# Kernel tuning notes

Hardware: AMD Instinct MI355X
Metric: run time of the kernel (lower is better)

## Reference

```python
import jax, jax.numpy as jnp
import numpy as np

B, S, D, H, FF = 2, 2048, 512, 8, 2048
DK = D // H
EPS = 1e-5


def layer_norm(x, g, b):
    mu = jnp.mean(x, axis=-1, keepdims=True)
    var = jnp.mean((x - mu) ** 2, axis=-1, keepdims=True)
    return (x - mu) / jnp.sqrt(var + EPS) * g + b


def split_heads(x):  # [B,S,D] -> [B,H,S,DK]
    b, s, _ = x.shape
    return x.reshape(b, s, H, DK).transpose(0, 2, 1, 3)


def merge_heads(x):  # [B,H,S,DK] -> [B,S,D]
    b, h, s, dk = x.shape
    return x.transpose(0, 2, 1, 3).reshape(b, s, h * dk)


def mha(q_in, kv, in_w, in_b, out_w, out_b):
    # torch nn.MultiheadAttention, batch_first, eval mode (no dropout)
    Wq, Wk, Wv = in_w[:D], in_w[D:2 * D], in_w[2 * D:]
    bq, bk, bv = in_b[:D], in_b[D:2 * D], in_b[2 * D:]
    q = split_heads(q_in @ Wq.T + bq)
    k = split_heads(kv @ Wk.T + bk)
    v = split_heads(kv @ Wv.T + bv)
    scores = jnp.einsum('bhqd,bhkd->bhqk', q, k) / jnp.sqrt(jnp.float32(DK))
    attn = jax.nn.softmax(scores, axis=-1)
    out = merge_heads(jnp.einsum('bhqk,bhkd->bhqd', attn, v))
    return out @ out_w.T + out_b


def setup_inputs() -> dict:
    key = jax.random.key(0)
    ks = jax.random.split(key, 32)
    p = lambda k, shape: (jax.random.normal(k, shape, jnp.float32) * 0.02)
    inp = {
        'x_q': jax.random.normal(ks[0], (B, S, D), jnp.float32),
        'x1': jax.random.normal(ks[1], (B, S, D), jnp.float32),
        'x2': jax.random.normal(ks[2], (B, S, D), jnp.float32),
        # causal self-attention projections (no output proj in original)
        'sa_wq': p(ks[3], (D, D)), 'sa_bq': jnp.zeros((D,), jnp.float32),
        'sa_wk': p(ks[4], (D, D)), 'sa_bk': jnp.zeros((D,), jnp.float32),
        'sa_wv': p(ks[5], (D, D)), 'sa_bv': jnp.zeros((D,), jnp.float32),
        'ln1_g': jnp.ones((D,), jnp.float32), 'ln1_b': jnp.zeros((D,), jnp.float32),
        # shared cross-attention (cross_attn used twice in forward)
        'mha_in_w': p(ks[6], (3 * D, D)), 'mha_in_b': jnp.zeros((3 * D,), jnp.float32),
        'mha_out_w': p(ks[7], (D, D)), 'mha_out_b': jnp.zeros((D,), jnp.float32),
        # shared add_norm2 (used twice)
        'ln2_g': jnp.ones((D,), jnp.float32), 'ln2_b': jnp.zeros((D,), jnp.float32),
        # FFN
        'ffn_w1': p(ks[8], (FF, D)), 'ffn_b1': jnp.zeros((FF,), jnp.float32),
        'ffn_w2': p(ks[9], (D, FF)), 'ffn_b2': jnp.zeros((D,), jnp.float32),
        # add_norm3 (final)
        'ln3_g': jnp.ones((D,), jnp.float32), 'ln3_b': jnp.zeros((D,), jnp.float32),
    }
    return inp


def reference(x_q, x1, x2, sa_wq, sa_bq, sa_wk, sa_bk, sa_wv, sa_bv,
              ln1_g, ln1_b, mha_in_w, mha_in_b, mha_out_w, mha_out_b,
              ln2_g, ln2_b, ffn_w1, ffn_b1, ffn_w2, ffn_b2, ln3_g, ln3_b):
    # --- causal self-attention (hand-rolled, masked_fill with -1e9) ---
    q = split_heads(x_q @ sa_wq.T + sa_bq)
    k = split_heads(x_q @ sa_wk.T + sa_bk)
    v = split_heads(x_q @ sa_wv.T + sa_bv)
    scores = jnp.einsum('bhqd,bhkd->bhqk', q, k) / jnp.sqrt(jnp.float32(DK))
    causal = jnp.tril(jnp.ones((S, S), dtype=bool))
    scores = jnp.where(causal[None, None], scores, jnp.float32(-1e9))
    attn = jax.nn.softmax(scores, axis=-1)
    y_sa = merge_heads(jnp.einsum('bhqk,bhkd->bhqd', attn, v))
    y = layer_norm(x_q + y_sa, ln1_g, ln1_b)
    # --- cross-attention 1 (shared weights) + shared add_norm2 ---
    yattn = mha(y, x1, mha_in_w, mha_in_b, mha_out_w, mha_out_b)
    yattn = layer_norm(y + yattn, ln2_g, ln2_b)
    # --- cross-attention 2 (SAME module/weights as cross-attn 1) ---
    yattn2 = mha(yattn, x2, mha_in_w, mha_in_b, mha_out_w, mha_out_b)
    yattn2 = layer_norm(yattn + yattn2, ln2_g, ln2_b)
    # --- FFN + add_norm3 ---
    h = jax.nn.relu(yattn2 @ ffn_w1.T + ffn_b1)
    ff = h @ ffn_w2.T + ffn_b2
    return layer_norm(yattn2 + ff, ln3_g, ln3_b)
```

## Files before the change

### kernel.cpp

```cpp
#include <hip/hip_runtime.h>
#include <hip/hip_bf16.h>

#define S_LEN 2048
#define DMODEL 512
#define NHEAD 8
#define DKH 64
#define FFDIM 2048
#define BATCH 2
#define NROWS (BATCH * S_LEN)

using bf16 = __hip_bfloat16;
typedef __bf16 bf16x8 __attribute__((ext_vector_type(8)));
typedef float floatx4 __attribute__((ext_vector_type(4)));
typedef float floatx16 __attribute__((ext_vector_type(16)));

__device__ inline unsigned short f2bf_bits(float f) {
    union { float f; unsigned u; } c; c.f = f;
    return (unsigned short)((c.u + 0x7FFFu + ((c.u >> 16) & 1u)) >> 16);
}
__device__ inline unsigned pack2bf(float a, float b) {
    return (unsigned)f2bf_bits(a) | ((unsigned)f2bf_bits(b) << 16);
}
__device__ inline unsigned pk2(float a, float b) {
    float2 f; f.x = a; f.y = b;
    __hip_bfloat162 h = __float22bfloat162_rn(f);
    return *(unsigned*)&h;
}

__device__ __forceinline__ void gload_lds16(const bf16* g, bf16* l) {
    __builtin_amdgcn_global_load_lds(
        (const __attribute__((address_space(1))) void*)(const void*)g,
        (__attribute__((address_space(3))) void*)(void*)l, 16, 0, 0);
}

struct CvtSeg { const float* s; bf16* d; int n4; };
struct CvtDesc { CvtSeg seg[12]; };

__launch_bounds__(256)
__global__ void cvt_f32_bf16(CvtDesc desc) {
    const CvtSeg sg = desc.seg[blockIdx.y];
    const int stride = gridDim.x * 256;
    for (int i = blockIdx.x * 256 + threadIdx.x; i < sg.n4; i += stride) {
        const float4 v = ((const float4*)sg.s)[i];
        uint2 o;
        o.x = pack2bf(v.x, v.y);
        o.y = pack2bf(v.z, v.w);
        ((uint2*)sg.d)[i] = o;
    }
}

struct Epi {
    bf16*  outB[3];
    float* outF[3];
    const float* bias[3];
    float scale[3];
    int shift;
    int relu;
};

template <int BM, int BN>
__launch_bounds__(256)
__global__ void gemm2(const bf16* __restrict__ A, const bf16* __restrict__ W,
                      Epi epi, int K)
{
    constexpr int WR = BM / 32;
    constexpr int WC = BN / 32;
    constexpr int SA = BM / 16;
    constexpr int SB = BN / 16;
    constexpr int NG = 2 * (SA + SB);

    __shared__ alignas(16) bf16 As[2][BM][32];
    __shared__ alignas(16) bf16 Bs[2][BN][32];

    const int t = threadIdx.x;
    const int w = t >> 6;
    const int lane = t & 63;
    const int r16 = lane & 15;
    const int quad = lane >> 4;
    const int wm = w >> 1, wn = w & 1;
    const int m0 = blockIdx.x * BM;
    const int n0 = blockIdx.y * BN;

    floatx4 acc[WR][WC];
#pragma unroll
    for (int i = 0; i < WR; i++)
#pragma unroll
        for (int j = 0; j < WC; j++)
#pragma unroll
            for (int e = 0; e < 4; e++) acc[i][j][e] = 0.0f;

    const int grow = lane >> 2;
    const int gcol = (lane & 3) * 8;

    for (int k0 = 0; k0 < K; k0 += 64) {
        __syncthreads();
#pragma unroll
        for (int s = 0; s < NG; s += 4) {
            int sg = s + w;
            int p = 0;
            if (sg >= SA + SB) { p = 1; sg -= SA + SB; }
            const bf16* src;
            bf16* dst;
            if (sg < SA) {
                src = A + (size_t)(m0 + sg * 16 + grow) * K + k0 + 32 * p + gcol;
                dst = &As[p][sg * 16][0] + lane * 8;
            } else {
                const int sb = sg - SA;
                src = W + (size_t)(n0 + sb * 16 + grow) * K + k0 + 32 * p + gcol;
                dst = &Bs[p][sb * 16][0] + lane * 8;
            }
            gload_lds16(src, dst);
        }
        __syncthreads();

        bf16x8 af[2][WR], bfr[2][WC];
#pragma unroll
        for (int p = 0; p < 2; p++) {
#pragma unroll
            for (int i = 0; i < WR; i++)
                af[p][i] = *(const bf16x8*)&As[p][wm * (BM / 2) + 16 * i + r16][quad * 8];
#pragma unroll
            for (int j = 0; j < WC; j++)
                bfr[p][j] = *(const bf16x8*)&Bs[p][wn * (BN / 2) + 16 * j + r16][quad * 8];
        }
#pragma unroll
        for (int p = 0; p < 2; p++)
#pragma unroll
            for (int i = 0; i < WR; i++)
#pragma unroll
                for (int j = 0; j < WC; j++)
                    acc[i][j] = __builtin_amdgcn_mfma_f32_16x16x32_bf16(af[p][i], bfr[p][j], acc[i][j], 0, 0, 0);
    }

    const int mask = (1 << epi.shift) - 1;
#pragma unroll
    for (int j = 0; j < WC; j++) {
        const int colb = n0 + wn * (BN / 2) + 16 * j;
        const int sel = __builtin_amdgcn_readfirstlane(colb >> epi.shift);
        const int lcol = (colb & mask) + r16;
        const int ldw = mask + 1;
        const float bv = epi.bias[sel] ? epi.bias[sel][lcol] : 0.0f;
        const float sc = epi.scale[sel];
        bf16* ob = epi.outB[sel];
        float* of = epi.outF[sel];
#pragma unroll
        for (int i = 0; i < WR; i++) {
            const int rowb = m0 + wm * (BM / 2) + 16 * i + 4 * quad;
#pragma unroll
            for (int e = 0; e < 4; e++) {
                float v = (acc[i][j][e] + bv) * sc;
                if (epi.relu) v = fmaxf(v, 0.0f);
                const size_t idx = (size_t)(rowb + e) * ldw + lcol;
                if (of) of[idx] = v;
                if (ob) ob[idx] = __float2bfloat16(v);
            }
        }
    }
}

#define PST 72

__launch_bounds__(256)
__global__ void attn_mfma(const bf16* __restrict__ Qh, const bf16* __restrict__ Kh,
                          const bf16* __restrict__ Vh,
                          float* __restrict__ outF, bf16* __restrict__ outB,
                          int causal)
{
    __shared__ alignas(16) bf16 Vt[2][64][PST];
    __shared__ alignas(16) bf16 Ps[4][32][PST];
    __shared__ float Msh[2][64][34];

    const int t = threadIdx.x;
    const int w = t >> 6;
    const int lane = t & 63;
    const int c32 = lane & 31;
    const int hi = lane >> 5;
    const int pair = t >> 7;
    const int qg = w & 1;
    const int pl = t & 127;
    const int bh = blockIdx.y;
    const int b = bh >> 3, h = bh & 7;
    const int q0 = blockIdx.x * 64;
    const size_t rowbase = (size_t)b * S_LEN;
    const int hoff = h * DKH;

    bf16x8 qf[4];
    {
        const bf16* qp = Qh + (rowbase + q0 + 32 * qg + c32) * DMODEL + hoff + 8 * hi;
#pragma unroll
        for (int tt = 0; tt < 4; tt++) qf[tt] = *(const bf16x8*)(qp + 16 * tt);
    }

    floatx16 o0, o1;
#pragma unroll
    for (int e = 0; e < 16; e++) { o0[e] = 0.0f; o1[e] = 0.0f; }
    float m = -3e38f, l = 0.0f;

    const int rq = pl & 15;
    const int c8 = ((pl >> 4) & 7) * 8;

    const int nchunk = causal ? (q0 / 64 + 1) : (S_LEN / 64);
    const int nIter = (nchunk + 1) >> 1;

    for (int it = 0; it < nIter; it++) {
        const int ch = 2 * it + pair;
        const bool active = ch < nchunk;
        const int kb = ch * 64;
        __syncthreads();
        if (active) {
            union { uint4 u; unsigned short s[8]; } r0, r1, r2, r3;
            const bf16* vb = Vh + (rowbase + kb + 4 * rq) * DMODEL + hoff + c8;
            r0.u = *(const uint4*)(vb);
            r1.u = *(const uint4*)(vb + DMODEL);
            r2.u = *(const uint4*)(vb + 2 * DMODEL);
            r3.u = *(const uint4*)(vb + 3 * DMODEL);
#pragma unroll
            for (int j = 0; j < 8; j++) {
                ushort4 pk = { r0.s[j], r1.s[j], r2.s[j], r3.s[j] };
                *(ushort4*)&Vt[pair][c8 + j][4 * rq] = pk;
            }
        }

        if (active) {
            floatx16 s0, s1;
#pragma unroll
            for (int e = 0; e < 16; e++) { s0[e] = 0.0f; s1[e] = 0.0f; }
            const bf16* kp = Kh + (rowbase + kb + c32) * DMODEL + hoff + 8 * hi;
#pragma unroll
            for (int tt = 0; tt < 4; tt++) {
                const bf16x8 k0 = *(const bf16x8*)(kp + 16 * tt);
                const bf16x8 k1 = *(const bf16x8*)(kp + (size_t)32 * DMODEL + 16 * tt);
                s0 = __builtin_amdgcn_mfma_f32_32x32x16_bf16(k0, qf[tt], s0, 0, 0, 0);
                s1 = __builtin_amdgcn_mfma_f32_32x32x16_bf16(k1, qf[tt], s1, 0, 0, 0);
            }

            if (causal && kb == q0) {
                const int qq = 32 * qg + c32;
#pragma unroll
                for (int r = 0; r < 16; r++) {
                    const int kl = (r & 3) + 8 * (r >> 2) + 4 * hi;
                    if (kl > qq) s0[r] = -3e38f;
                    if (kl + 32 > qq) s1[r] = -3e38f;
                }
            }

            float mc = -3e38f;
#pragma unroll
            for (int r = 0; r < 16; r++) mc = fmaxf(mc, fmaxf(s0[r], s1[r]));
            mc = fmaxf(mc, __shfl_xor(mc, 32, 64));
            const float mold = m;
            const float mn = fmaxf(m, mc);
            const float alpha = __expf(mold - mn);
            m = mn;

            float lc = 0.0f;
#pragma unroll
            for (int g = 0; g < 4; g++) {
                float p0 = __expf(s0[4 * g + 0] - mn), p1 = __expf(s0[4 * g + 1] - mn);
                float p2 = __expf(s0[4 * g + 2] - mn), p3 = __expf(s0[4 * g + 3] - mn);
                lc += (p0 + p1) + (p2 + p3);
                uint2 pw; pw.x = pk2(p0, p1); pw.y = pk2(p2, p3);
                *(uint2*)&Ps[w][c32][8 * g + 4 * hi] = pw;
                p0 = __expf(s1[4 * g + 0] - mn); p1 = __expf(s1[4 * g + 1] - mn);
                p2 = __expf(s1[4 * g + 2] - mn); p3 = __expf(s1[4 * g + 3] - mn);
                lc += (p0 + p1) + (p2 + p3);
                uint2 pw1; pw1.x = pk2(p0, p1); pw1.y = pk2(p2, p3);
                *(uint2*)&Ps[w][c32][32 + 8 * g + 4 * hi] = pw1;
            }
            lc += __shfl_xor(lc, 32, 64);
            l = l * alpha + lc;

            if (!__all(mn == mold)) {
#pragma unroll
                for (int r = 0; r < 16; r++) {
                    const float a = __shfl(alpha, (r & 3) + 8 * (r >> 2) + 4 * hi, 64);
                    o0[r] *= a; o1[r] *= a;
                }
            }
        }

        __syncthreads();

        if (active) {
#pragma unroll
            for (int tt = 0; tt < 4; tt++) {
                const bf16x8 pf = *(const bf16x8*)&Ps[w][c32][16 * tt + 8 * hi];
                const bf16x8 v0 = *(const bf16x8*)&Vt[pair][c32][16 * tt + 8 * hi];
                const bf16x8 v1 = *(const bf16x8*)&Vt[pair][32 + c32][16 * tt + 8 * hi];
                o0 = __builtin_amdgcn_mfma_f32_32x32x16_bf16(pf, v0, o0, 0, 0, 0);
                o1 = __builtin_amdgcn_mfma_f32_32x32x16_bf16(pf, v1, o1, 0, 0, 0);
            }
        }
    }

    __syncthreads();
    if (pair == 1) {
        float* dst = &Msh[qg][lane][0];
        dst[0] = m; dst[1] = l;
#pragma unroll
        for (int r = 0; r < 16; r++) { dst[2 + r] = o0[r]; dst[18 + r] = o1[r]; }
    }
    __syncthreads();
    if (pair == 0) {
        const float* src = &Msh[qg][lane][0];
        const float m_b = src[0], l_b = src[1];
        const float mt = fmaxf(m, m_b);
        const float sA = __expf(m - mt);
        const float sB = __expf(m_b - mt);
        const float lt = l * sA + l_b * sB;
#pragma unroll
        for (int r = 0; r < 16; r++) {
            const int ql = (r & 3) + 8 * (r >> 2) + 4 * hi;
            const float sAr = __shfl(sA, ql, 64);
            const float sBr = __shfl(sB, ql, 64);
            const float li = 1.0f / __shfl(lt, ql, 64);
            const float v0 = (o0[r] * sAr + src[2 + r] * sBr) * li;
            const float v1 = (o1[r] * sAr + src[18 + r] * sBr) * li;
            const size_t idx = (rowbase + q0 + 32 * qg + ql) * DMODEL + hoff + c32;
            if (outF) { outF[idx] = v0; outF[idx + 32] = v1; }
            if (outB) { outB[idx] = __float2bfloat16(v0); outB[idx + 32] = __float2bfloat16(v1); }
        }
    }
}

__launch_bounds__(256)
__global__ void ln_kernel(const float* __restrict__ xmain,
                          const float* __restrict__ resF, const bf16* __restrict__ resB,
                          const float* __restrict__ g, const float* __restrict__ bb,
                          float* __restrict__ outF, bf16* __restrict__ outB)
{
    const int row = blockIdx.x;
    const int t = threadIdx.x;
    const size_t base = (size_t)row * DMODEL;

    float x0 = xmain[base + t];
    float x1 = xmain[base + t + 256];
    if (resF) { x0 += resF[base + t]; x1 += resF[base + t + 256]; }
    if (resB) { x0 += __bfloat162float(resB[base + t]); x1 += __bfloat162float(resB[base + t + 256]); }

    __shared__ float sred[4];
    float s = x0 + x1;
#pragma unroll
    for (int off = 32; off > 0; off >>= 1) s += __shfl_down(s, off);
    if ((t & 63) == 0) sred[t >> 6] = s;
    __syncthreads();
    const float mu = (sred[0] + sred[1] + sred[2] + sred[3]) * (1.0f / DMODEL);

    const float d0 = x0 - mu, d1 = x1 - mu;
    float sv = d0 * d0 + d1 * d1;
#pragma unroll
    for (int off = 32; off > 0; off >>= 1) sv += __shfl_down(sv, off);
    __syncthreads();
    if ((t & 63) == 0) sred[t >> 6] = sv;
    __syncthreads();
    const float var = (sred[0] + sred[1] + sred[2] + sred[3]) * (1.0f / DMODEL);
    const float rstd = rsqrtf(var + 1e-5f);

    const float y0 = d0 * rstd * g[t] + bb[t];
    const float y1 = d1 * rstd * g[t + 256] + bb[t + 256];
    if (outF) { outF[base + t] = y0; outF[base + t + 256] = y1; }
    if (outB) { outB[base + t] = __float2bfloat16(y0); outB[base + t + 256] = __float2bfloat16(y1); }
}

extern "C" void kernel_launch(void* const* d_in, const int* in_sizes, int n_in,
                              void* d_out, int out_size, void* d_ws, size_t ws_size,
                              hipStream_t stream)
{
    const float* x_q       = (const float*)d_in[0];
    const float* x1        = (const float*)d_in[1];
    const float* x2        = (const float*)d_in[2];
    const float* sa_wq     = (const float*)d_in[3];
    const float* sa_bq     = (const float*)d_in[4];
    const float* sa_wk     = (const float*)d_in[5];
    const float* sa_bk     = (const float*)d_in[6];
    const float* sa_wv     = (const float*)d_in[7];
    const float* sa_bv     = (const float*)d_in[8];
    const float* ln1_g     = (const float*)d_in[9];
    const float* ln1_b     = (const float*)d_in[10];
    const float* mha_in_w  = (const float*)d_in[11];
    const float* mha_in_b  = (const float*)d_in[12];
    const float* mha_out_w = (const float*)d_in[13];
    const float* mha_out_b = (const float*)d_in[14];
    const float* ln2_g     = (const float*)d_in[15];
    const float* ln2_b     = (const float*)d_in[16];
    const float* ffn_w1    = (const float*)d_in[17];
    const float* ffn_b1    = (const float*)d_in[18];
    const float* ffn_w2    = (const float*)d_in[19];
    const float* ffn_b2    = (const float*)d_in[20];
    const float* ln3_g     = (const float*)d_in[21];
    const float* ln3_b     = (const float*)d_in[22];

    char* ws = (char*)d_ws;
    const size_t MB = 1024 * 1024;
    const size_t KB = 1024;
    bf16*  q16  = (bf16*)(ws + 0 * MB);
    bf16*  k16  = (bf16*)(ws + 4 * MB);
    bf16*  v16  = (bf16*)(ws + 8 * MB);
    bf16*  a16  = (bf16*)(ws + 12 * MB);
    float* tmp  = (float*)(ws + 16 * MB);
    bf16*  y16  = (bf16*)(ws + 24 * MB);
    bf16*  ya16 = (bf16*)(ws + 28 * MB);
    bf16*  ya2  = (bf16*)(ws + 32 * MB);
    bf16*  xq16 = (bf16*)(ws + 36 * MB);
    bf16*  x116 = (bf16*)(ws + 40 * MB);
    bf16*  x216 = (bf16*)(ws + 44 * MB);
    bf16*  w_sa_qkv = (bf16*)(ws + 48 * MB);
    bf16*  w_in   = (bf16*)(ws + 49 * MB + 512 * KB);
    bf16*  w_out  = (bf16*)(ws + 51 * MB);
    bf16*  w_f1   = (bf16*)(ws + 51 * MB + 512 * KB);
    bf16*  w_f2   = (bf16*)(ws + 53 * MB + 512 * KB);
    bf16*  h16    = (bf16*)(ws + 0 * MB);

    const int DD = DMODEL * DMODEL;
    CvtDesc cd;
    cd.seg[0]  = { x_q,       xq16,        (NROWS * DMODEL) / 4 };
    cd.seg[1]  = { x1,        x116,        (NROWS * DMODEL) / 4 };
    cd.seg[2]  = { x2,        x216,        (NROWS * DMODEL) / 4 };
    cd.seg[3]  = { sa_wq,     w_sa_qkv,           DD / 4 };
    cd.seg[4]  = { sa_wk,     w_sa_qkv + DD,      DD / 4 };
    cd.seg[5]  = { sa_wv,     w_sa_qkv + 2 * DD,  DD / 4 };
    cd.seg[6]  = { mha_in_w,  w_in,   3 * DD / 4 };
    cd.seg[7]  = { mha_out_w, w_out,  DD / 4 };
    cd.seg[8]  = { ffn_w1,    w_f1,   (FFDIM * DMODEL) / 4 };
    cd.seg[9]  = { ffn_w2,    w_f2,   (FFDIM * DMODEL) / 4 };
    cd.seg[10] = { x_q,       xq16,   0 };
    cd.seg[11] = { x_q,       xq16,   0 };
    cvt_f32_bf16<<<dim3(64, 10), 256, 0, stream>>>(cd);

    const dim3 blk(256);
    const dim3 agrid(S_LEN / 64, BATCH * NHEAD);

    Epi eQKV = {};
    eQKV.outB[0] = q16; eQKV.outB[1] = k16; eQKV.outB[2] = v16;
    eQKV.bias[0] = sa_bq; eQKV.bias[1] = sa_bk; eQKV.bias[2] = sa_bv;
    eQKV.scale[0] = 0.125f; eQKV.scale[1] = 1.0f; eQKV.scale[2] = 1.0f;
    eQKV.shift = 9;

    Epi eQ = {};
    eQ.outB[0] = q16; eQ.bias[0] = mha_in_b; eQ.scale[0] = 0.125f; eQ.shift = 9;

    Epi eKV = {};
    eKV.outB[0] = k16; eKV.outB[1] = v16;
    eKV.bias[0] = mha_in_b + DMODEL; eKV.bias[1] = mha_in_b + 2 * DMODEL;
    eKV.scale[0] = 1.0f; eKV.scale[1] = 1.0f; eKV.shift = 9;

    Epi eOut = {};
    eOut.outF[0] = tmp; eOut.bias[0] = mha_out_b; eOut.scale[0] = 1.0f; eOut.shift = 9;

    Epi eF1 = {};
    eF1.outB[0] = h16; eF1.bias[0] = ffn_b1; eF1.scale[0] = 1.0f;
    eF1.shift = 11; eF1.relu = 1;

    Epi eF2 = {};
    eF2.outF[0] = tmp; eF2.bias[0] = ffn_b2; eF2.scale[0] = 1.0f; eF2.shift = 9;

    gemm2<64, 64><<<dim3(64, 24), blk, 0, stream>>>(xq16, w_sa_qkv, eQKV, DMODEL);
    attn_mfma<<<agrid, blk, 0, stream>>>(q16, k16, v16, tmp, nullptr, 1);
    ln_kernel<<<NROWS, blk, 0, stream>>>(tmp, x_q, nullptr, ln1_g, ln1_b, nullptr, y16);

    gemm2<64, 64><<<dim3(64, 8), blk, 0, stream>>>(y16, w_in, eQ, DMODEL);
    gemm2<64, 64><<<dim3(64, 16), blk, 0, stream>>>(x116, w_in + (size_t)DD, eKV, DMODEL);
    attn_mfma<<<agrid, blk, 0, stream>>>(q16, k16, v16, nullptr, a16, 0);
    gemm2<64, 64><<<dim3(64, 8), blk, 0, stream>>>(a16, w_out, eOut, DMODEL);
    ln_kernel<<<NROWS, blk, 0, stream>>>(tmp, nullptr, y16, ln2_g, ln2_b, nullptr, ya16);

    gemm2<64, 64><<<dim3(64, 8), blk, 0, stream>>>(ya16, w_in, eQ, DMODEL);
    gemm2<64, 64><<<dim3(64, 16), blk, 0, stream>>>(x216, w_in + (size_t)DD, eKV, DMODEL);
    attn_mfma<<<agrid, blk, 0, stream>>>(q16, k16, v16, nullptr, a16, 0);
    gemm2<64, 64><<<dim3(64, 8), blk, 0, stream>>>(a16, w_out, eOut, DMODEL);
    ln_kernel<<<NROWS, blk, 0, stream>>>(tmp, nullptr, ya16, ln2_g, ln2_b, nullptr, ya2);

    gemm2<128, 128><<<dim3(32, 16), blk, 0, stream>>>(ya2, w_f1, eF1, DMODEL);
    gemm2<64, 64><<<dim3(64, 8), blk, 0, stream>>>(h16, w_f2, eF2, FFDIM);
    ln_kernel<<<NROWS, blk, 0, stream>>>(tmp, nullptr, ya2, ln3_g, ln3_b, (float*)d_out, nullptr);
}
```

Before: 458.4 us.

## Fuse cross-attn Q/KV projections into one GEMM and prefetch K tiles in attention

The GEMM gains an alternate A pointer that is selected per N-slab, so the Q projection (from y) and the K/V projections (from x1/x2) run in a single 24-column-block launch instead of two launches. The attention kernel now loads the next K chunk into registers while the current chunk's scores are processed, hiding global-load latency behind the MFMA and softmax work. Shared memory is aliased into one buffer so the Msh scratch overlaps Vt/Ps, which lowers LDS use. The cost is more registers held for the prefetched K fragments, and a correctness risk if the Msh phase overlaps live Vt/Ps data.

```diff
diff --git a/kernel.cpp b/kernel.cpp
--- a/kernel.cpp
+++ b/kernel.cpp
@@ -54,6 +54,8 @@
     float* outF[3];
     const float* bias[3];
     float scale[3];
+    const bf16* A2;
+    int a2slab;
     int shift;
     int relu;
 };
@@ -81,6 +83,8 @@
     const int m0 = blockIdx.x * BM;
     const int n0 = blockIdx.y * BN;
 
+    const bf16* Ause = (epi.A2 && ((n0 >> epi.shift) >= epi.a2slab)) ? epi.A2 : A;
+
     floatx4 acc[WR][WC];
 #pragma unroll
     for (int i = 0; i < WR; i++)
@@ -102,7 +106,7 @@
             const bf16* src;
             bf16* dst;
             if (sg < SA) {
-                src = A + (size_t)(m0 + sg * 16 + grow) * K + k0 + 32 * p + gcol;
+                src = Ause + (size_t)(m0 + sg * 16 + grow) * K + k0 + 32 * p + gcol;
                 dst = &As[p][sg * 16][0] + lane * 8;
             } else {
                 const int sb = sg - SA;
@@ -166,9 +170,13 @@
                           float* __restrict__ outF, bf16* __restrict__ outB,
                           int causal)
 {
-    __shared__ alignas(16) bf16 Vt[2][64][PST];
-    __shared__ alignas(16) bf16 Ps[4][32][PST];
-    __shared__ float Msh[2][64][34];
+    __shared__ alignas(16) char smem[36864];
+    typedef bf16 (*VtT)[64][PST];
+    typedef bf16 (*PsT)[32][PST];
+    VtT Vt = (VtT)smem;
+    PsT Ps = (PsT)(smem + 18432);
+    typedef float (*MshT)[64][34];
+    MshT Msh = (MshT)smem;
 
     const int t = threadIdx.x;
     const int w = t >> 6;
@@ -202,6 +210,16 @@
     const int nchunk = causal ? (q0 / 64 + 1) : (S_LEN / 64);
     const int nIter = (nchunk + 1) >> 1;
 
+    bf16x8 kf0[4], kf1[4];
+    if (pair < nchunk) {
+        const bf16* kp = Kh + (rowbase + pair * 64 + c32) * DMODEL + hoff + 8 * hi;
+#pragma unroll
+        for (int tt = 0; tt < 4; tt++) {
+            kf0[tt] = *(const bf16x8*)(kp + 16 * tt);
+            kf1[tt] = *(const bf16x8*)(kp + (size_t)32 * DMODEL + 16 * tt);
+        }
+    }
+
     for (int it = 0; it < nIter; it++) {
         const int ch = 2 * it + pair;
         const bool active = ch < nchunk;
@@ -225,13 +243,20 @@
             floatx16 s0, s1;
 #pragma unroll
             for (int e = 0; e < 16; e++) { s0[e] = 0.0f; s1[e] = 0.0f; }
-            const bf16* kp = Kh + (rowbase + kb + c32) * DMODEL + hoff + 8 * hi;
 #pragma unroll
             for (int tt = 0; tt < 4; tt++) {
-                const bf16x8 k0 = *(const bf16x8*)(kp + 16 * tt);
-                const bf16x8 k1 = *(const bf16x8*)(kp + (size_t)32 * DMODEL + 16 * tt);
-                s0 = __builtin_amdgcn_mfma_f32_32x32x16_bf16(k0, qf[tt], s0, 0, 0, 0);
-                s1 = __builtin_amdgcn_mfma_f32_32x32x16_bf16(k1, qf[tt], s1, 0, 0, 0);
+                s0 = __builtin_amdgcn_mfma_f32_32x32x16_bf16(kf0[tt], qf[tt], s0, 0, 0, 0);
+                s1 = __builtin_amdgcn_mfma_f32_32x32x16_bf16(kf1[tt], qf[tt], s1, 0, 0, 0);
+            }
+
+            const int chn = ch + 2;
+            if (chn < nchunk) {
+                const bf16* kp = Kh + (rowbase + chn * 64 + c32) * DMODEL + hoff + 8 * hi;
+#pragma unroll
+                for (int tt = 0; tt < 4; tt++) {
+                    kf0[tt] = *(const bf16x8*)(kp + 16 * tt);
+                    kf1[tt] = *(const bf16x8*)(kp + (size_t)32 * DMODEL + 16 * tt);
+                }
             }
 
             if (causal && kb == q0) {
@@ -436,13 +461,14 @@
     eQKV.scale[0] = 0.125f; eQKV.scale[1] = 1.0f; eQKV.scale[2] = 1.0f;
     eQKV.shift = 9;
 
-    Epi eQ = {};
-    eQ.outB[0] = q16; eQ.bias[0] = mha_in_b; eQ.scale[0] = 0.125f; eQ.shift = 9;
-
-    Epi eKV = {};
-    eKV.outB[0] = k16; eKV.outB[1] = v16;
-    eKV.bias[0] = mha_in_b + DMODEL; eKV.bias[1] = mha_in_b + 2 * DMODEL;
-    eKV.scale[0] = 1.0f; eKV.scale[1] = 1.0f; eKV.shift = 9;
+    Epi eX1 = {};
+    eX1.outB[0] = q16; eX1.outB[1] = k16; eX1.outB[2] = v16;
+    eX1.bias[0] = mha_in_b; eX1.bias[1] = mha_in_b + DMODEL; eX1.bias[2] = mha_in_b + 2 * DMODEL;
+    eX1.scale[0] = 0.125f; eX1.scale[1] = 1.0f; eX1.scale[2] = 1.0f;
+    eX1.A2 = x116; eX1.a2slab = 1; eX1.shift = 9;
+
+    Epi eX2 = eX1;
+    eX2.A2 = x216;
 
     Epi eOut = {};
     eOut.outF[0] = tmp; eOut.bias[0] = mha_out_b; eOut.scale[0] = 1.0f; eOut.shift = 9;
@@ -458,14 +484,12 @@
     attn_mfma<<<agrid, blk, 0, stream>>>(q16, k16, v16, tmp, nullptr, 1);
     ln_kernel<<<NROWS, blk, 0, stream>>>(tmp, x_q, nullptr, ln1_g, ln1_b, nullptr, y16);
 
-    gemm2<64, 64><<<dim3(64, 8), blk, 0, stream>>>(y16, w_in, eQ, DMODEL);
-    gemm2<64, 64><<<dim3(64, 16), blk, 0, stream>>>(x116, w_in + (size_t)DD, eKV, DMODEL);
+    gemm2<64, 64><<<dim3(64, 24), blk, 0, stream>>>(y16, w_in, eX1, DMODEL);
     attn_mfma<<<agrid, blk, 0, stream>>>(q16, k16, v16, nullptr, a16, 0);
     gemm2<64, 64><<<dim3(64, 8), blk, 0, stream>>>(a16, w_out, eOut, DMODEL);
     ln_kernel<<<NROWS, blk, 0, stream>>>(tmp, nullptr, y16, ln2_g, ln2_b, nullptr, ya16);
 
-    gemm2<64, 64><<<dim3(64, 8), blk, 0, stream>>>(ya16, w_in, eQ, DMODEL);
-    gemm2<64, 64><<<dim3(64, 16), blk, 0, stream>>>(x216, w_in + (size_t)DD, eKV, DMODEL);
+    gemm2<64, 64><<<dim3(64, 24), blk, 0, stream>>>(ya16, w_in, eX2, DMODEL);
     attn_mfma<<<agrid, blk, 0, stream>>>(q16, k16, v16, nullptr, a16, 0);
     gemm2<64, 64><<<dim3(64, 8), blk, 0, stream>>>(a16, w_out, eOut, DMODEL);
     ln_kernel<<<NROWS, blk, 0, stream>>>(tmp, nullptr, ya16, ln2_g, ln2_b, nullptr, ya2);
```

Result: faster. 441.3 us (-3.7%).
